# Kernel tuning notes

Hardware: AMD Instinct MI355X
Metric: run time of the kernel (lower is better)

The kernel has to match this reference:

```python
import jax, jax.numpy as jnp
import numpy as np
from jax import lax

B, T, HW = 8, 32, 128
D, NH, DEPTH, DFF = 384, 6, 6, 1536
PR = PC = 4
P = PR * PC
EPS = 1e-5


def _ln(x, g, b):
    mu = x.mean(-1, keepdims=True)
    v = ((x - mu) ** 2).mean(-1, keepdims=True)
    return (x - mu) / jnp.sqrt(v + EPS) * g + b


def _conv2d(x, w, s, p):
    return lax.conv_general_dilated(x, w, (s, s), [(p, p), (p, p)],
                                    dimension_numbers=('NCHW', 'OIHW', 'NCHW'))


def _bn(x, g, b, m, v):
    inv = g / jnp.sqrt(v + EPS)
    return x * inv[:, None, None] + (b - m * inv)[:, None, None]


def _gelu(x):
    return jax.nn.gelu(x, approximate=False)


def _forward(frames, conv1_w, bn1_g, bn1_b, bn1_m, bn1_v,
             conv2_w, bn2_g, bn2_b, bn2_m, bn2_v,
             conv3_w, bn3_g, bn3_b, bn3_m, bn3_v, proj_w,
             dw_w, dw_b, pw_w, pw_b, tnorm_g, tnorm_b,
             frame_pos, patch_pos, cls_token, cls_pos,
             qkv_w, qkv_b, out_w, out_b, ln1_g, ln1_b, ln2_g, ln2_b,
             ffn_w1, ffn_b1, ffn_w2, ffn_b2,
             head_ln_g, head_ln_b, head_w1, head_b1, head_w2, head_b2):
    b, t = frames.shape[0], frames.shape[1]
    # ---- FrameEncoder (eval-mode BN) ----
    x = frames.reshape(b * t, 1, HW, HW)
    x = _gelu(_bn(_conv2d(x, conv1_w, 2, 2), bn1_g, bn1_b, bn1_m, bn1_v))
    x = _gelu(_bn(_conv2d(x, conv2_w, 2, 1), bn2_g, bn2_b, bn2_m, bn2_v))
    x = _gelu(_bn(_conv2d(x, conv3_w, 2, 1), bn3_g, bn3_b, bn3_m, bn3_v))
    n, c, hh, ww = x.shape
    # adaptive avg pool (16,16)->(4,4) is an exact 4x4 mean pool
    x = x.reshape(n, c, PR, hh // PR, PC, ww // PC).mean(axis=(3, 5))
    x = jnp.einsum('oc,nchw->nohw', proj_w[:, :, 0, 0], x)  # 1x1 conv proj
    tokens = x.reshape(n, D, P).transpose(0, 2, 1).reshape(b, t, P, D)
    # ---- TemporalConvBlock (per-patch sequences) ----
    tc = tokens.transpose(0, 2, 1, 3).reshape(b * P, t, D)
    out = tc.transpose(0, 2, 1)  # [N, D, t]
    for i, dil in enumerate((1, 2)):
        pad = dil * (3 - 1) // 2
        h = lax.conv_general_dilated(out, dw_w[i], (1,), [(pad, pad)],
                                     rhs_dilation=(dil,), feature_group_count=D,
                                     dimension_numbers=('NCH', 'OIH', 'NCH'))
        h = _gelu(h + dw_b[i][None, :, None])
        h = jnp.einsum('oi,nit->not', pw_w[i], h) + pw_b[i][None, :, None]
        out = h + out
    out = out.transpose(0, 2, 1)
    tc = _ln(out + tc, tnorm_g, tnorm_b)
    tokens = tc.reshape(b, P, t, D).transpose(0, 2, 1, 3)
    # ---- positional + cls ----
    fp = frame_pos[:t].transpose(1, 0, 2)[:, :, None, :]  # [1,t,1,D]
    pp = patch_pos[:, None, :, :]                          # [1,1,P,D]
    tok = (tokens + fp + pp).reshape(b, t * P, D)
    cls = cls_token + cls_pos
    tok = jnp.concatenate([jnp.broadcast_to(cls, (b, 1, D)), tok], axis=1)
    S = t * P + 1
    # ---- block-structured additive mask (faithful to _build_causal_mask) ----
    ids = jnp.repeat(jnp.arange(t), P)
    neg = jnp.finfo(jnp.float32).min
    base = jnp.where(ids[None, :] < ids[:, None], neg, 0.0)
    mask = jnp.zeros((S, S), jnp.float32).at[1:, 1:].set(base).at[1:, 0].set(neg)
    # ---- pre-norm transformer encoder ----
    hd = D // NH
    scale = 1.0 / jnp.sqrt(jnp.float32(hd))
    x = tok
    for i in range(DEPTH):
        h = _ln(x, ln1_g[i], ln1_b[i])
        qkv = h @ qkv_w[i].T + qkv_b[i]
        q, k, v = jnp.split(qkv, 3, axis=-1)
        q = q.reshape(b, S, NH, hd).transpose(0, 2, 1, 3)
        k = k.reshape(b, S, NH, hd).transpose(0, 2, 1, 3)
        v = v.reshape(b, S, NH, hd).transpose(0, 2, 1, 3)
        scores = jnp.einsum('bhqd,bhkd->bhqk', q, k) * scale + mask
        a = jax.nn.softmax(scores, axis=-1)
        o = jnp.einsum('bhqk,bhkd->bhqd', a, v).transpose(0, 2, 1, 3).reshape(b, S, D)
        x = x + (o @ out_w[i].T + out_b[i])
        h2 = _ln(x, ln2_g[i], ln2_b[i])
        x = x + _gelu(h2 @ ffn_w1[i].T + ffn_b1[i]) @ ffn_w2[i].T + ffn_b2[i]
    # ---- coord head ----
    pooled = x[:, 0]
    h = _ln(pooled, head_ln_g, head_ln_b)
    h = _gelu(h @ head_w1.T + head_b1)
    coords = jax.nn.sigmoid(h @ head_w2.T + head_b2)
    return coords


def setup_inputs():
    ks = iter(jax.random.split(jax.random.key(0), 64))

    def r(shape, s):
        return jax.random.normal(next(ks), shape, jnp.float32) * s

    inp = {}
    inp['frames'] = jax.random.normal(next(ks), (B, T, 1, HW, HW), jnp.float32)
    inp['conv1_w'] = r((32, 1, 5, 5), 0.2)
    inp['bn1_g'] = jnp.ones(32); inp['bn1_b'] = jnp.zeros(32)
    inp['bn1_m'] = r((32,), 0.1)
    inp['bn1_v'] = jax.random.uniform(next(ks), (32,), jnp.float32, 0.5, 1.5)
    inp['conv2_w'] = r((64, 32, 3, 3), 0.1)
    inp['bn2_g'] = jnp.ones(64); inp['bn2_b'] = jnp.zeros(64)
    inp['bn2_m'] = r((64,), 0.1)
    inp['bn2_v'] = jax.random.uniform(next(ks), (64,), jnp.float32, 0.5, 1.5)
    inp['conv3_w'] = r((128, 64, 3, 3), 0.07)
    inp['bn3_g'] = jnp.ones(128); inp['bn3_b'] = jnp.zeros(128)
    inp['bn3_m'] = r((128,), 0.1)
    inp['bn3_v'] = jax.random.uniform(next(ks), (128,), jnp.float32, 0.5, 1.5)
    inp['proj_w'] = r((D, 128, 1, 1), 0.08)
    inp['dw_w'] = r((2, D, 1, 3), 0.3)
    inp['dw_b'] = jnp.zeros((2, D))
    inp['pw_w'] = r((2, D, D), 0.05)
    inp['pw_b'] = jnp.zeros((2, D))
    inp['tnorm_g'] = jnp.ones(D); inp['tnorm_b'] = jnp.zeros(D)
    inp['frame_pos'] = r((T, 1, D), 0.02)
    inp['patch_pos'] = r((1, P, D), 0.02)
    inp['cls_token'] = jnp.zeros((1, 1, D))
    inp['cls_pos'] = r((1, 1, D), 0.02)
    inp['qkv_w'] = r((DEPTH, 3 * D, D), 0.02)
    inp['qkv_b'] = jnp.zeros((DEPTH, 3 * D))
    inp['out_w'] = r((DEPTH, D, D), 0.02)
    inp['out_b'] = jnp.zeros((DEPTH, D))
    inp['ln1_g'] = jnp.ones((DEPTH, D)); inp['ln1_b'] = jnp.zeros((DEPTH, D))
    inp['ln2_g'] = jnp.ones((DEPTH, D)); inp['ln2_b'] = jnp.zeros((DEPTH, D))
    inp['ffn_w1'] = r((DEPTH, DFF, D), 0.02)
    inp['ffn_b1'] = jnp.zeros((DEPTH, DFF))
    inp['ffn_w2'] = r((DEPTH, D, DFF), 0.02)
    inp['ffn_b2'] = jnp.zeros((DEPTH, D))
    inp['head_ln_g'] = jnp.ones(D); inp['head_ln_b'] = jnp.zeros(D)
    inp['head_w1'] = r((D, D), 0.02); inp['head_b1'] = jnp.zeros(D)
    inp['head_w2'] = r((2, D), 0.02); inp['head_b2'] = jnp.zeros(2)
    return inp


def reference(frames, conv1_w, bn1_g, bn1_b, bn1_m, bn1_v,
              conv2_w, bn2_g, bn2_b, bn2_m, bn2_v,
              conv3_w, bn3_g, bn3_b, bn3_m, bn3_v, proj_w,
              dw_w, dw_b, pw_w, pw_b, tnorm_g, tnorm_b,
              frame_pos, patch_pos, cls_token, cls_pos,
              qkv_w, qkv_b, out_w, out_b, ln1_g, ln1_b, ln2_g, ln2_b,
              ffn_w1, ffn_b1, ffn_w2, ffn_b2,
              head_ln_g, head_ln_b, head_w1, head_b1, head_w2, head_b2):
    return _forward(frames, conv1_w, bn1_g, bn1_b, bn1_m, bn1_v,
                    conv2_w, bn2_g, bn2_b, bn2_m, bn2_v,
                    conv3_w, bn3_g, bn3_b, bn3_m, bn3_v, proj_w,
                    dw_w, dw_b, pw_w, pw_b, tnorm_g, tnorm_b,
                    frame_pos, patch_pos, cls_token, cls_pos,
                    qkv_w, qkv_b, out_w, out_b, ln1_g, ln1_b, ln2_g, ln2_b,
                    ffn_w1, ffn_b1, ffn_w2, ffn_b2,
                    head_ln_g, head_ln_b, head_w1, head_b1, head_w2, head_b2)
```

## Files before the change

kernel.cpp:

```cpp
#include <hip/hip_runtime.h>
#include <hip/hip_fp16.h>
#include <cstddef>

#define EPSV 1e-5f

typedef _Float16 f16;
typedef _Float16 f16x8 __attribute__((ext_vector_type(8)));
typedef float f32x4v __attribute__((ext_vector_type(4)));

__device__ __forceinline__ float gelu_f(float x) {
    return 0.5f * x * (1.0f + erff(x * 0.7071067811865476f));
}

__device__ __forceinline__ float gelu_fast(float x) {
    float y = 0.7978845608f * (x + 0.044715f * x * x * x);
    y = fminf(fmaxf(y, -10.f), 10.f);
    float e = __expf(2.f * y);
    float t = (e - 1.f) / (e + 1.f);
    return 0.5f * x * (1.f + t);
}

__global__ __launch_bounds__(256) void cvt_all_kernel(
    const float* __restrict__ p0, const float* __restrict__ p1,
    const float* __restrict__ p2, const float* __restrict__ p3,
    const float* __restrict__ p4, const float* __restrict__ p5,
    f16* __restrict__ dst)
{
    const int n = 10960896;
    for (int i = blockIdx.x * 256 + threadIdx.x; i < n; i += gridDim.x * 256) {
        const float* s; int off;
        if      (i <   49152) { s = p0; off = i; }
        else if (i <  344064) { s = p1; off = i -   49152; }
        else if (i < 2998272) { s = p2; off = i -  344064; }
        else if (i < 3883008) { s = p3; off = i - 2998272; }
        else if (i < 7421952) { s = p4; off = i - 3883008; }
        else                  { s = p5; off = i - 7421952; }
        dst[i] = (f16)s[off];
    }
}

__global__ __launch_bounds__(256) void conv_w_reorder_kernel(
    const float* __restrict__ w, f16* __restrict__ out, int CO, int CI)
{
    int n = CO * CI * 9;
    for (int i = blockIdx.x * 256 + threadIdx.x; i < n; i += gridDim.x * 256) {
        int t = i % 9; int r = i / 9;
        int ci = r % CI; int co = r / CI;
        out[(size_t)co * CI * 9 + t * CI + ci] = (f16)w[i];
    }
}

__global__ __launch_bounds__(256) void conv1_w_prep_kernel(
    const float* __restrict__ w, const float* __restrict__ g,
    const float* __restrict__ vr, f16* __restrict__ wB)
{
    int i = blockIdx.x * 256 + threadIdx.x;
    if (i >= 1024) return;
    int co = i >> 5, k = i & 31;
    float inv = g[co] * rsqrtf(vr[co] + EPSV);
    wB[i] = (f16)((k < 25) ? w[co * 25 + k] * inv : 0.f);
}

__global__ __launch_bounds__(256) void conv1_mfma_kernel(
    const float* __restrict__ in, const f16* __restrict__ wB,
    const float* __restrict__ bt, const float* __restrict__ mn,
    const float* __restrict__ g, const float* __restrict__ vr,
    f16* __restrict__ out)
{
    __shared__ __align__(16) f16 inpH[35 * 36 + 8];
    __shared__ __align__(16) f16 Bs[32 * 32];
    int bid = blockIdx.x;
    int n = bid >> 4; int tile = bid & 15;
    int ty0 = (tile >> 2) * 16, tx0 = (tile & 3) * 16;
    int t = threadIdx.x;
    const float* ip = in + (size_t)n * 16384;
    for (int e = t; e < 35 * 36; e += 256) {
        int r = e / 36, c = e - r * 36;
        int iy = ty0 * 2 - 2 + r, ix = tx0 * 2 - 2 + c;
        float v = ((unsigned)iy < 128u && (unsigned)ix < 128u && c < 35) ? ip[iy * 128 + ix] : 0.f;
        inpH[e] = (f16)v;
    }
    if (t < 128) {
        int row = t >> 2, seg = (t & 3) * 8;
        *(uint4*)(&Bs[row * 32 + seg]) = *(const uint4*)(wB + row * 32 + seg);
    }
    __syncthreads();
    int w = t >> 6, lane = t & 63;
    int l15 = lane & 15, gq = lane >> 4;
    f16x8 afr[4];
    #pragma unroll
    for (int i = 0; i < 4; i++) {
        int mt = 4 * w + i;
        f16 tmp[8];
        #pragma unroll
        for (int e = 0; e < 8; e++) {
            int kk = 8 * gq + e; if (kk > 24) kk = 24;
            int ky = kk / 5, kx = kk - ky * 5;
            tmp[e] = inpH[(2 * mt + ky) * 36 + 2 * l15 + kx];
        }
        afr[i] = *(f16x8*)tmp;
    }
    f16x8 bfr[2];
    bfr[0] = *(const f16x8*)(&Bs[l15 * 32 + 8 * gq]);
    bfr[1] = *(const f16x8*)(&Bs[(16 + l15) * 32 + 8 * gq]);
    f32x4v zero = {0.f, 0.f, 0.f, 0.f};
    f32x4v acc[4][2];
    #pragma unroll
    for (int i = 0; i < 4; i++) { acc[i][0] = zero; acc[i][1] = zero; }
    #pragma unroll
    for (int i = 0; i < 4; i++) {
        acc[i][0] = __builtin_amdgcn_mfma_f32_16x16x32_f16(afr[i], bfr[0], acc[i][0], 0, 0, 0);
        acc[i][1] = __builtin_amdgcn_mfma_f32_16x16x32_f16(afr[i], bfr[1], acc[i][1], 0, 0, 0);
    }
    float beta[2];
    #pragma unroll
    for (int nt = 0; nt < 2; nt++) {
        int co = nt * 16 + l15;
        float inv = g[co] * rsqrtf(vr[co] + EPSV);
        beta[nt] = bt[co] - mn[co] * inv;
    }
    #pragma unroll
    for (int i = 0; i < 4; i++) {
        int y = ty0 + 4 * w + i;
        #pragma unroll
        for (int q = 0; q < 4; q++) {
            int x = tx0 + 4 * gq + q;
            size_t ob = (((size_t)n * 64 + y) * 64 + x) * 32;
            #pragma unroll
            for (int nt = 0; nt < 2; nt++) {
                int co = nt * 16 + l15;
                out[ob + co] = (f16)gelu_fast(acc[i][nt][q] + beta[nt]);
            }
        }
    }
}

template<int CI, int HI, int CO>
__global__ __launch_bounds__(256) void convg_kernel(
    const f16* __restrict__ in, const f16* __restrict__ wr_,
    const float* __restrict__ g, const float* __restrict__ bt,
    const float* __restrict__ mn, const float* __restrict__ vr,
    f16* __restrict__ out)
{
    constexpr int HO = HI / 2;
    constexpr int HOB = (HO == 32) ? 5 : 4;
    constexpr int K = 9 * CI;
    __shared__ __align__(16) f16 As[64 * 40];
    __shared__ __align__(16) f16 Bs[64 * 40];
    int tid = threadIdx.x;
    int bm = blockIdx.x * 64;
    int bn = blockIdx.y * 64;
    int lrow = tid >> 2, lseg = tid & 3;
    int w = tid >> 6, lane = tid & 63;
    int wr = (w >> 1) * 32, wc = (w & 1) * 32;
    int l15 = lane & 15, l4 = lane >> 4;
    int gp = bm + lrow;
    int pn = gp >> (2 * HOB);
    int prem = gp & ((1 << (2 * HOB)) - 1);
    int oy = prem >> HOB, ox = prem & (HO - 1);

    f32x4v zero = {0.f, 0.f, 0.f, 0.f};
    f32x4v acc[2][2];
    acc[0][0] = zero; acc[0][1] = zero; acc[1][0] = zero; acc[1][1] = zero;

    auto loadTile = [&](int k0, uint4& av, uint4& bv) {
        int tap = k0 / CI;
        int cio = k0 - tap * CI;
        int ky = tap / 3, kx = tap - ky * 3;
        int iy = oy * 2 - 1 + ky, ix = ox * 2 - 1 + kx;
        av = make_uint4(0u, 0u, 0u, 0u);
        if ((unsigned)iy < (unsigned)HI && (unsigned)ix < (unsigned)HI)
            av = *(const uint4*)(in + (((size_t)(pn * HI + iy)) * HI + ix) * CI + cio + lseg * 8);
        bv = *(const uint4*)(wr_ + (size_t)(bn + lrow) * K + k0 + lseg * 8);
    };

    uint4 ra, rb;
    loadTile(0, ra, rb);
    for (int k0 = 0; k0 < K; k0 += 32) {
        __syncthreads();
        *(uint4*)(&As[lrow * 40 + lseg * 8]) = ra;
        *(uint4*)(&Bs[lrow * 40 + lseg * 8]) = rb;
        if (k0 + 32 < K) loadTile(k0 + 32, ra, rb);
        __syncthreads();
        f16x8 a0 = *(const f16x8*)(&As[(wr + l15) * 40 + l4 * 8]);
        f16x8 a1 = *(const f16x8*)(&As[(wr + 16 + l15) * 40 + l4 * 8]);
        f16x8 b0 = *(const f16x8*)(&Bs[(wc + l15) * 40 + l4 * 8]);
        f16x8 b1 = *(const f16x8*)(&Bs[(wc + 16 + l15) * 40 + l4 * 8]);
        acc[0][0] = __builtin_amdgcn_mfma_f32_16x16x32_f16(a0, b0, acc[0][0], 0, 0, 0);
        acc[0][1] = __builtin_amdgcn_mfma_f32_16x16x32_f16(a0, b1, acc[0][1], 0, 0, 0);
        acc[1][0] = __builtin_amdgcn_mfma_f32_16x16x32_f16(a1, b0, acc[1][0], 0, 0, 0);
        acc[1][1] = __builtin_amdgcn_mfma_f32_16x16x32_f16(a1, b1, acc[1][1], 0, 0, 0);
    }
    float inv[2], beta[2];
    #pragma unroll
    for (int ni = 0; ni < 2; ni++) {
        int col = bn + wc + ni * 16 + l15;
        float iv = g[col] * rsqrtf(vr[col] + EPSV);
        inv[ni] = iv; beta[ni] = bt[col] - mn[col] * iv;
    }
    #pragma unroll
    for (int mi = 0; mi < 2; mi++) {
        #pragma unroll
        for (int q = 0; q < 4; q++) {
            int pixel = bm + wr + mi * 16 + l4 * 4 + q;
            #pragma unroll
            for (int ni = 0; ni < 2; ni++) {
                int col = bn + wc + ni * 16 + l15;
                float v = acc[mi][ni][q] * inv[ni] + beta[ni];
                out[(size_t)pixel * CO + col] = (f16)gelu_fast(v);
            }
        }
    }
}

__global__ __launch_bounds__(256) void poolh_kernel(
    const f16* __restrict__ in, f16* __restrict__ out, int NC)
{
    int idx = blockIdx.x * 256 + threadIdx.x;
    if (idx >= NC * 16 * 16) return;
    int cc = idx & 15; int npl = idx >> 4;
    int c0 = cc * 8;
    int n = npl >> 4; int p = npl & 15;
    int ph = p >> 2, pw = p & 3;
    const f16* base = in + (((size_t)(n * 16 + ph * 4)) * 16 + pw * 4) * 128 + c0;
    float s[8] = {};
    #pragma unroll
    for (int dy = 0; dy < 4; dy++)
        #pragma unroll
        for (int dx = 0; dx < 4; dx++) {
            f16x8 v = *(const f16x8*)(base + (dy * 16 + dx) * 128);
            #pragma unroll
            for (int u = 0; u < 8; u++) s[u] += (float)v[u];
        }
    f16* op = out + (size_t)npl * 128 + c0;
    #pragma unroll
    for (int u = 0; u < 8; u++) op[u] = (f16)(s[u] * 0.0625f);
}

template<int OUTF16, int ACT, int VTRANS>
__global__ __launch_bounds__(256) void gemm_k64_kernel(
    const f16* __restrict__ A, const f16* __restrict__ B,
    const float* __restrict__ bias, const float* __restrict__ res,
    void* __restrict__ Cv, f16* __restrict__ vT, int M, int N, int K, int nrow)
{
    __shared__ __align__(16) f16 As[64 * 72];
    __shared__ __align__(16) f16 Bs[64 * 72];
    int nb = gridDim.x;
    int q = nb >> 3, r = nb & 7;
    int xcd = blockIdx.x & 7, pos = blockIdx.x >> 3;
    int logical = (xcd < r ? xcd * (q + 1) : r * (q + 1) + (xcd - r) * q) + pos;
    int brow = logical % nrow, bcol = logical / nrow;
    int bm = brow * 64, bn = bcol * 64;

    int tid = threadIdx.x;
    int lrow = tid >> 2, lseg = (tid & 3) * 16;
    int w = tid >> 6, lane = tid & 63;
    int wr = (w >> 1) * 32, wc = (w & 1) * 32;
    int l15 = lane & 15, l4 = lane >> 4;
    f32x4v zero = {0.f, 0.f, 0.f, 0.f};
    f32x4v acc[2][2];
    acc[0][0] = zero; acc[0][1] = zero; acc[1][0] = zero; acc[1][1] = zero;

    int arow = bm + lrow;
    bool aok = (arow < M);
    const f16* ap = A + (size_t)arow * K + lseg;
    const f16* bp = B + (size_t)(bn + lrow) * K + lseg;

    uint4 ra0 = make_uint4(0u,0u,0u,0u), ra1 = ra0, rb0, rb1;
    if (aok) { ra0 = *(const uint4*)(ap); ra1 = *(const uint4*)(ap + 8); }
    rb0 = *(const uint4*)(bp); rb1 = *(const uint4*)(bp + 8);

    int nt = K >> 6;
    for (int t = 0; t < nt; t++) {
        __syncthreads();
        *(uint4*)(&As[lrow * 72 + lseg])     = ra0;
        *(uint4*)(&As[lrow * 72 + lseg + 8]) = ra1;
        *(uint4*)(&Bs[lrow * 72 + lseg])     = rb0;
        *(uint4*)(&Bs[lrow * 72 + lseg + 8]) = rb1;
        if (t + 1 < nt) {
            int k0 = (t + 1) << 6;
            if (aok) { ra0 = *(const uint4*)(ap + k0); ra1 = *(const uint4*)(ap + k0 + 8); }
            rb0 = *(const uint4*)(bp + k0); rb1 = *(const uint4*)(bp + k0 + 8);
        }
        __syncthreads();
        #pragma unroll
        for (int s = 0; s < 2; s++) {
            f16x8 a0 = *(const f16x8*)(&As[(wr + l15) * 72 + s * 32 + l4 * 8]);
            f16x8 a1 = *(const f16x8*)(&As[(wr + 16 + l15) * 72 + s * 32 + l4 * 8]);
            f16x8 b0 = *(const f16x8*)(&Bs[(wc + l15) * 72 + s * 32 + l4 * 8]);
            f16x8 b1 = *(const f16x8*)(&Bs[(wc + 16 + l15) * 72 + s * 32 + l4 * 8]);
            acc[0][0] = __builtin_amdgcn_mfma_f32_16x16x32_f16(a0, b0, acc[0][0], 0, 0, 0);
            acc[0][1] = __builtin_amdgcn_mfma_f32_16x16x32_f16(a0, b1, acc[0][1], 0, 0, 0);
            acc[1][0] = __builtin_amdgcn_mfma_f32_16x16x32_f16(a1, b0, acc[1][0], 0, 0, 0);
            acc[1][1] = __builtin_amdgcn_mfma_f32_16x16x32_f16(a1, b1, acc[1][1], 0, 0, 0);
        }
    }

    if (VTRANS && bn >= 768) {
        __syncthreads();
        f16* tile = As;
        #pragma unroll
        for (int mi = 0; mi < 2; mi++)
            #pragma unroll
            for (int qq = 0; qq < 4; qq++) {
                int rl = wr + mi * 16 + l4 * 4 + qq;
                #pragma unroll
                for (int ni = 0; ni < 2; ni++) {
                    int dl = wc + ni * 16 + l15;
                    float v = acc[mi][ni][qq] + bias[bn + dl];
                    tile[dl * 66 + rl] = (f16)v;
                }
            }
        __syncthreads();
        int h = (bn - 768) >> 6;
        int j = tid & 63, dbase = tid >> 6;
        int trow = bm + j;
        if (trow < M) {
            int b = trow / 513;
            int jj = trow - b * 513;
            f16* vb = vT + ((size_t)(b * 6 + h) * 64) * 576 + jj;
            #pragma unroll
            for (int it = 0; it < 16; it++) {
                int d = dbase * 16 + it;
                vb[(size_t)d * 576] = tile[d * 66 + j];
            }
        }
        return;
    }
    #pragma unroll
    for (int mi = 0; mi < 2; mi++) {
        #pragma unroll
        for (int qq = 0; qq < 4; qq++) {
            int row = bm + wr + mi * 16 + l4 * 4 + qq;
            if (row >= M) continue;
            #pragma unroll
            for (int ni = 0; ni < 2; ni++) {
                int col = bn + wc + ni * 16 + l15;
                float v = acc[mi][ni][qq];
                if (bias) v += bias[col];
                if (ACT == 1) v = gelu_fast(v);
                if (res) v += res[(size_t)row * N + col];
                if (OUTF16) ((f16*)Cv)[(size_t)row * N + col] = (f16)v;
                else ((float*)Cv)[(size_t)row * N + col] = v;
            }
        }
    }
}

template<int ACT>
__global__ __launch_bounds__(256) void gemm_kn128_kernel(
    const f16* __restrict__ A, const f16* __restrict__ B,
    const float* __restrict__ bias, f16* __restrict__ C,
    int M, int N, int K, int nrow)
{
    __shared__ __align__(16) f16 As[64 * 72];
    __shared__ __align__(16) f16 Bs[128 * 72];
    int nb = gridDim.x;
    int q = nb >> 3, r = nb & 7;
    int xcd = blockIdx.x & 7, pos = blockIdx.x >> 3;
    int logical = (xcd < r ? xcd * (q + 1) : r * (q + 1) + (xcd - r) * q) + pos;
    int brow = logical % nrow, bcol = logical / nrow;
    int bm = brow * 64, bn = bcol * 128;

    int tid = threadIdx.x;
    int w = tid >> 6, lane = tid & 63;
    int wr = (w >> 1) * 32, wc = (w & 1) * 64;
    int l15 = lane & 15, l4 = lane >> 4;
    int alrow = tid >> 2, alseg = (tid & 3) * 16;
    int blrow = tid >> 1, blseg = (tid & 1) * 32;

    f32x4v zero = {0.f, 0.f, 0.f, 0.f};
    f32x4v acc[2][4];
    #pragma unroll
    for (int i = 0; i < 2; i++)
        #pragma unroll
        for (int j = 0; j < 4; j++) acc[i][j] = zero;

    int arow = bm + alrow;
    bool aok = (arow < M);
    const f16* ap = A + (size_t)arow * K + alseg;
    const f16* bp = B + (size_t)(bn + blrow) * K + blseg;

    uint4 ra0 = make_uint4(0u,0u,0u,0u), ra1 = ra0;
    uint4 rb0, rb1, rb2, rb3;
    if (aok) { ra0 = *(const uint4*)(ap); ra1 = *(const uint4*)(ap + 8); }
    rb0 = *(const uint4*)(bp);      rb1 = *(const uint4*)(bp + 8);
    rb2 = *(const uint4*)(bp + 16); rb3 = *(const uint4*)(bp + 24);

    int ntiles = K >> 6;
    for (int t = 0; t < ntiles; t++) {
        __syncthreads();
        *(uint4*)(&As[alrow * 72 + alseg])     = ra0;
        *(uint4*)(&As[alrow * 72 + alseg + 8]) = ra1;
        *(uint4*)(&Bs[blrow * 72 + blseg])      = rb0;
        *(uint4*)(&Bs[blrow * 72 + blseg + 8])  = rb1;
        *(uint4*)(&Bs[blrow * 72 + blseg + 16]) = rb2;
        *(uint4*)(&Bs[blrow * 72 + blseg + 24]) = rb3;
        if (t + 1 < ntiles) {
            int k0 = (t + 1) << 6;
            if (aok) { ra0 = *(const uint4*)(ap + k0); ra1 = *(const uint4*)(ap + k0 + 8); }
            rb0 = *(const uint4*)(bp + k0);      rb1 = *(const uint4*)(bp + k0 + 8);
            rb2 = *(const uint4*)(bp + k0 + 16); rb3 = *(const uint4*)(bp + k0 + 24);
        }
        __syncthreads();
        #pragma unroll
        for (int s = 0; s < 2; s++) {
            f16x8 a0 = *(const f16x8*)(&As[(wr + l15) * 72 + s * 32 + l4 * 8]);
            f16x8 a1 = *(const f16x8*)(&As[(wr + 16 + l15) * 72 + s * 32 + l4 * 8]);
            #pragma unroll
            for (int j = 0; j < 4; j++) {
                f16x8 bf = *(const f16x8*)(&Bs[(wc + j * 16 + l15) * 72 + s * 32 + l4 * 8]);
                acc[0][j] = __builtin_amdgcn_mfma_f32_16x16x32_f16(a0, bf, acc[0][j], 0, 0, 0);
                acc[1][j] = __builtin_amdgcn_mfma_f32_16x16x32_f16(a1, bf, acc[1][j], 0, 0, 0);
            }
        }
    }
    #pragma unroll
    for (int mi = 0; mi < 2; mi++) {
        #pragma unroll
        for (int qq = 0; qq < 4; qq++) {
            int row = bm + wr + mi * 16 + l4 * 4 + qq;
            if (row >= M) continue;
            #pragma unroll
            for (int j = 0; j < 4; j++) {
                int col = bn + wc + j * 16 + l15;
                float v = acc[mi][j][qq];
                if (bias) v += bias[col];
                if (ACT == 1) v = gelu_fast(v);
                C[(size_t)row * N + col] = (f16)v;
            }
        }
    }
}

__global__ __launch_bounds__(256) void tok2tc_kernel(
    const float* __restrict__ in, float* __restrict__ out)
{
    int idx = blockIdx.x * 256 + threadIdx.x;
    if (idx >= 8 * 32 * 16 * 384) return;
    int d = idx % 384; int t2 = idx / 384;
    int p = t2 & 15; t2 >>= 4;
    int t = t2 & 31; int b = t2 >> 5;
    out[(((size_t)(b * 16 + p) * 32 + t) * 384) + d] = in[idx];
}

__global__ __launch_bounds__(256) void dwconv_kernel(
    const float* __restrict__ in, const float* __restrict__ w,
    const float* __restrict__ bias, f16* __restrict__ out, int dil)
{
    int idx = blockIdx.x * 256 + threadIdx.x;
    if (idx >= 128 * 32 * 384) return;
    int d = idx % 384; int t = (idx / 384) & 31; int s = idx / (384 * 32);
    const float* ip = in + (size_t)s * 32 * 384 + d;
    float acc = bias[d];
    #pragma unroll
    for (int k = 0; k < 3; k++) {
        int tt = t + (k - 1) * dil;
        if ((unsigned)tt < 32u) acc += w[d * 3 + k] * ip[tt * 384];
    }
    out[idx] = (f16)gelu_fast(acc);
}

__global__ __launch_bounds__(256) void ln_wave_kernel(
    const float* __restrict__ in,
    const float* __restrict__ g, const float* __restrict__ b,
    f16* __restrict__ out, int rows)
{
    int w = threadIdx.x >> 6, lane = threadIdx.x & 63;
    int row = blockIdx.x * 4 + w;
    if (row >= rows) return;
    const float* ip = in + (size_t)row * 384;
    float x[6]; float s = 0.f, s2 = 0.f;
    #pragma unroll
    for (int k = 0; k < 6; k++) {
        float v = ip[lane + 64 * k];
        x[k] = v; s += v; s2 += v * v;
    }
    #pragma unroll
    for (int off = 1; off < 64; off <<= 1) {
        s += __shfl_xor(s, off); s2 += __shfl_xor(s2, off);
    }
    float mu = s * (1.f / 384.f);
    float var = s2 * (1.f / 384.f) - mu * mu;
    float rs = rsqrtf(var + EPSV);
    #pragma unroll
    for (int k = 0; k < 6; k++) {
        int c = lane + 64 * k;
        out[(size_t)row * 384 + c] = (f16)((x[k] - mu) * rs * g[c] + b[c]);
    }
}

__global__ __launch_bounds__(128) void build_x_kernel(
    const float* __restrict__ mix, const float* __restrict__ tc,
    const float* __restrict__ tg, const float* __restrict__ tb,
    const float* __restrict__ fpos, const float* __restrict__ ppos,
    float* __restrict__ x)
{
    int row = blockIdx.x;
    int t = row & 31; int bp = row >> 5;
    int p = bp & 15; int b = bp >> 4;
    int tid = threadIdx.x;
    const float* ip = mix + (size_t)row * 384;
    const float* ip2 = tc + (size_t)row * 384;
    __shared__ float red[128], red2[128];
    float v[3]; float s = 0.f, s2 = 0.f;
    #pragma unroll
    for (int j = 0; j < 3; j++) {
        float val = ip[tid + 128 * j] + ip2[tid + 128 * j];
        v[j] = val; s += val; s2 += val * val;
    }
    red[tid] = s; red2[tid] = s2; __syncthreads();
    for (int off = 64; off >= 1; off >>= 1) {
        if (tid < off) { red[tid] += red[tid + off]; red2[tid] += red2[tid + off]; }
        __syncthreads();
    }
    float mu = red[0] * (1.f / 384.f);
    float var = red2[0] * (1.f / 384.f) - mu * mu;
    float rs = rsqrtf(var + EPSV);
    size_t xbase = ((size_t)b * 513 + 1 + t * 16 + p) * 384;
    #pragma unroll
    for (int j = 0; j < 3; j++) {
        int c = tid + 128 * j;
        float y = (v[j] - mu) * rs * tg[c] + tb[c] + fpos[t * 384 + c] + ppos[p * 384 + c];
        x[xbase + c] = y;
    }
}

__global__ __launch_bounds__(256) void cls_kernel(
    const float* __restrict__ ct, const float* __restrict__ cp, float* __restrict__ x)
{
    int idx = blockIdx.x * 256 + threadIdx.x;
    if (idx >= 8 * 384) return;
    int c = idx % 384; int b = idx / 384;
    x[(size_t)b * 513 * 384 + c] = ct[c] + cp[c];
}

__global__ __launch_bounds__(256) void fattn_split_kernel(
    const f16* __restrict__ qkv, const f16* __restrict__ vT,
    f16* __restrict__ Op, float* __restrict__ ml)
{
    __shared__ __align__(16) f16 Pl[4][16][72];
    int qt = blockIdx.x;
    int bh = blockIdx.y; int h = bh % 6; int b = bh / 6;
    int third = blockIdx.z;
    int tid = threadIdx.x;
    int w = tid >> 6, lane = tid & 63;
    int l15 = lane & 15, g = lane >> 4;
    int q0w = qt * 64 + w * 16;
    if (q0w > 512) return;
    const size_t RS = 1152;
    const f16* qbase = qkv + (size_t)b * 513 * RS + h * 64;
    const f16* kbase = qbase + 384;
    const f16* vtb = vT + (size_t)bh * 64 * 576;

    f16x8 qf[2];
    {
        int qrow = q0w + l15; if (qrow > 512) qrow = 512;
        const f16* qp = qbase + (size_t)qrow * RS + g * 8;
        qf[0] = *(const f16x8*)(qp);
        qf[1] = *(const f16x8*)(qp + 32);
    }

    f32x4v zero = {0.f, 0.f, 0.f, 0.f};
    f32x4v O[4]; float m[4], l[4];
    #pragma unroll
    for (int i = 0; i < 4; i++) { O[i] = zero; m[i] = -INFINITY; l[i] = 0.f; }

    int jt0 = 0;
    if (q0w > 0) { int fmin = (q0w - 1) >> 4; jt0 = (fmin * 16 + 1) >> 6; }

    int jrow[4];
    #pragma unroll
    for (int jf = 0; jf < 4; jf++) jrow[jf] = jf * 16 + l15;

    auto loadK = [&](int j0, f16x8* kr) {
        #pragma unroll
        for (int s = 0; s < 2; s++)
            #pragma unroll
            for (int jf = 0; jf < 4; jf++) {
                int j = j0 + jrow[jf]; if (j > 512) j = 512;
                kr[s * 4 + jf] = *(const f16x8*)(kbase + (size_t)j * RS + s * 32 + g * 8);
            }
    };

    int jt = jt0 + third;
    f16x8 kreg[8];
    if (jt < 9) loadK(jt * 64, kreg);

    for (; jt < 9; jt += 3) {
        int j0 = jt * 64;
        f16x8 vreg[8];
        #pragma unroll
        for (int s = 0; s < 2; s++)
            #pragma unroll
            for (int df = 0; df < 4; df++)
                vreg[s * 4 + df] = *(const f16x8*)(vtb + (size_t)(df * 16 + l15) * 576 + j0 + s * 32 + g * 8);
        f32x4v S[4];
        #pragma unroll
        for (int jf = 0; jf < 4; jf++) S[jf] = zero;
        #pragma unroll
        for (int s = 0; s < 2; s++)
            #pragma unroll
            for (int jf = 0; jf < 4; jf++)
                S[jf] = __builtin_amdgcn_mfma_f32_16x16x32_f16(qf[s], kreg[s * 4 + jf], S[jf], 0, 0, 0);
        f16x8 knext[8];
        if (jt + 3 < 9) loadK((jt + 3) * 64, knext);
        float pj[4][4];
        #pragma unroll
        for (int r = 0; r < 4; r++) {
            int qi = q0w + 4 * g + r;
            int fi = (qi == 0) ? -1 : ((qi - 1) >> 4);
            float mx = -INFINITY;
            #pragma unroll
            for (int jf = 0; jf < 4; jf++) {
                int j = j0 + jrow[jf];
                bool valid = (qi < 513) && (j < 513) &&
                             !((qi != 0) && ((j == 0) || (((j - 1) >> 4) < fi)));
                float sv = valid ? S[jf][r] * 0.125f : -INFINITY;
                pj[jf][r] = sv;
                mx = fmaxf(mx, sv);
            }
            mx = fmaxf(mx, __shfl_xor(mx, 1));
            mx = fmaxf(mx, __shfl_xor(mx, 2));
            mx = fmaxf(mx, __shfl_xor(mx, 4));
            mx = fmaxf(mx, __shfl_xor(mx, 8));
            float mn = fmaxf(m[r], mx);
            float alpha = (m[r] == -INFINITY) ? 0.f : __expf(m[r] - mn);
            float ls = 0.f;
            #pragma unroll
            for (int jf = 0; jf < 4; jf++) {
                float p = (pj[jf][r] == -INFINITY) ? 0.f : __expf(pj[jf][r] - mn);
                pj[jf][r] = p; ls += p;
            }
            ls += __shfl_xor(ls, 1); ls += __shfl_xor(ls, 2);
            ls += __shfl_xor(ls, 4); ls += __shfl_xor(ls, 8);
            l[r] = alpha * l[r] + ls;
            m[r] = mn;
            #pragma unroll
            for (int df = 0; df < 4; df++) O[df][r] *= alpha;
        }
        #pragma unroll
        for (int jf = 0; jf < 4; jf++)
            #pragma unroll
            for (int r = 0; r < 4; r++)
                Pl[w][4 * g + r][jf * 16 + l15] = (f16)pj[jf][r];
        #pragma unroll
        for (int s = 0; s < 2; s++) {
            f16x8 pf = *(const f16x8*)(&Pl[w][l15][s * 32 + g * 8]);
            #pragma unroll
            for (int df = 0; df < 4; df++)
                O[df] = __builtin_amdgcn_mfma_f32_16x16x32_f16(pf, vreg[s * 4 + df], O[df], 0, 0, 0);
        }
        #pragma unroll
        for (int i = 0; i < 8; i++) kreg[i] = knext[i];
    }

    int rowbase = third * 24624 + bh * 513;
    #pragma unroll
    for (int r = 0; r < 4; r++) {
        int qi = q0w + 4 * g + r;
        if (qi > 512) continue;
        size_t ro = (size_t)(rowbase + qi);
        #pragma unroll
        for (int df = 0; df < 4; df++)
            Op[ro * 64 + df * 16 + l15] = (f16)O[df][r];
        if (l15 == 0) {
            ml[ro * 2 + 0] = m[r];
            ml[ro * 2 + 1] = l[r];
        }
    }
}

__global__ __launch_bounds__(256) void attn_combine_kernel(
    const f16* __restrict__ Op, const float* __restrict__ ml,
    f16* __restrict__ ob)
{
    int row = blockIdx.x * 4 + (threadIdx.x >> 6);
    if (row >= 24624) return;
    int lane = threadIdx.x & 63;
    int bh = row / 513, qi = row - bh * 513;
    int b = bh / 6, h = bh - b * 6;
    float mv[3], lv[3], mm = -INFINITY;
    #pragma unroll
    for (int s = 0; s < 3; s++) {
        mv[s] = ml[((size_t)s * 24624 + row) * 2];
        lv[s] = ml[((size_t)s * 24624 + row) * 2 + 1];
        mm = fmaxf(mm, mv[s]);
    }
    float onum = 0.f, lden = 0.f;
    #pragma unroll
    for (int s = 0; s < 3; s++) {
        float a = (mv[s] == -INFINITY) ? 0.f : __expf(mv[s] - mm);
        lden += lv[s] * a;
        onum += (float)Op[((size_t)s * 24624 + row) * 64 + lane] * a;
    }
    ob[((size_t)(b * 513 + qi)) * 384 + h * 64 + lane] = (f16)(onum / lden);
}

__global__ __launch_bounds__(384) void head_kernel(
    const float* __restrict__ x, const float* __restrict__ lg, const float* __restrict__ lb,
    const float* __restrict__ w1, const float* __restrict__ b1,
    const float* __restrict__ w2, const float* __restrict__ b2,
    float* __restrict__ out)
{
    int b = blockIdx.x; int t = threadIdx.x;
    __shared__ float hs[384], h1[384];
    __shared__ float rs[6], rs2[6];
    const float* xp = x + (size_t)b * 513 * 384;
    float v = xp[t];
    float s = v, s2 = v * v;
    #pragma unroll
    for (int off = 32; off >= 1; off >>= 1) {
        s += __shfl_down(s, off); s2 += __shfl_down(s2, off);
    }
    if ((t & 63) == 0) { rs[t >> 6] = s; rs2[t >> 6] = s2; }
    __syncthreads();
    float S = 0.f, S2 = 0.f;
    #pragma unroll
    for (int i = 0; i < 6; i++) { S += rs[i]; S2 += rs2[i]; }
    float mu = S * (1.f / 384.f);
    float var = S2 * (1.f / 384.f) - mu * mu;
    float rstd = rsqrtf(var + EPSV);
    hs[t] = (v - mu) * rstd * lg[t] + lb[t];
    __syncthreads();
    const float* wr = w1 + (size_t)t * 384;
    float acc = b1[t];
    for (int c = 0; c < 384; c += 4) {
        float4 w4 = *reinterpret_cast<const float4*>(wr + c);
        acc += w4.x * hs[c] + w4.y * hs[c + 1] + w4.z * hs[c + 2] + w4.w * hs[c + 3];
    }
    h1[t] = gelu_f(acc);
    __syncthreads();
    float p0 = h1[t] * w2[t], p1 = h1[t] * w2[384 + t];
    #pragma unroll
    for (int off = 32; off >= 1; off >>= 1) {
        p0 += __shfl_down(p0, off); p1 += __shfl_down(p1, off);
    }
    if ((t & 63) == 0) { rs[t >> 6] = p0; rs2[t >> 6] = p1; }
    __syncthreads();
    if (t == 0) {
        float a0 = b2[0], a1 = b2[1];
        #pragma unroll
        for (int i = 0; i < 6; i++) { a0 += rs[i]; a1 += rs2[i]; }
        out[b * 2 + 0] = 1.f / (1.f + expf(-a0));
        out[b * 2 + 1] = 1.f / (1.f + expf(-a1));
    }
}

static inline int cdiv(int a, int b) { return (a + b - 1) / b; }

extern "C" void kernel_launch(void* const* d_in, const int* in_sizes, int n_in,
                              void* d_out, int out_size, void* d_ws, size_t ws_size,
                              hipStream_t stream)
{
    const float* frames  = (const float*)d_in[0];
    const float* conv1_w = (const float*)d_in[1];
    const float* bn1_g = (const float*)d_in[2]; const float* bn1_b = (const float*)d_in[3];
    const float* bn1_m = (const float*)d_in[4]; const float* bn1_v = (const float*)d_in[5];
    const float* conv2_w = (const float*)d_in[6];
    const float* bn2_g = (const float*)d_in[7]; const float* bn2_b = (const float*)d_in[8];
    const float* bn2_m = (const float*)d_in[9]; const float* bn2_v = (const float*)d_in[10];
    const float* conv3_w = (const float*)d_in[11];
    const float* bn3_g = (const float*)d_in[12]; const float* bn3_b = (const float*)d_in[13];
    const float* bn3_m = (const float*)d_in[14]; const float* bn3_v = (const float*)d_in[15];
    const float* proj_w = (const float*)d_in[16];
    const float* dw_w = (const float*)d_in[17]; const float* dw_b = (const float*)d_in[18];
    const float* pw_w = (const float*)d_in[19]; const float* pw_b = (const float*)d_in[20];
    const float* tnorm_g = (const float*)d_in[21]; const float* tnorm_b = (const float*)d_in[22];
    const float* frame_pos = (const float*)d_in[23];
    const float* patch_pos = (const float*)d_in[24];
    const float* cls_token = (const float*)d_in[25];
    const float* cls_pos = (const float*)d_in[26];
    const float* qkv_w = (const float*)d_in[27]; const float* qkv_b = (const float*)d_in[28];
    const float* out_w = (const float*)d_in[29]; const float* out_b = (const float*)d_in[30];
    const float* ln1_g = (const float*)d_in[31]; const float* ln1_b = (const float*)d_in[32];
    const float* ln2_g = (const float*)d_in[33]; const float* ln2_b = (const float*)d_in[34];
    const float* ffn_w1 = (const float*)d_in[35]; const float* ffn_b1 = (const float*)d_in[36];
    const float* ffn_w2 = (const float*)d_in[37]; const float* ffn_b2 = (const float*)d_in[38];
    const float* head_ln_g = (const float*)d_in[39]; const float* head_ln_b = (const float*)d_in[40];
    const float* head_w1 = (const float*)d_in[41]; const float* head_b1 = (const float*)d_in[42];
    const float* head_w2 = (const float*)d_in[43]; const float* head_b2 = (const float*)d_in[44];
    (void)in_sizes; (void)n_in; (void)out_size; (void)ws_size;

    char* base = (char*)d_ws;
    size_t off = 0;
    auto alloc = [&](size_t bytes) { void* p = base + off; off = (off + bytes + 255) & ~(size_t)255; return p; };

    f16* wtotal = (f16*)alloc((size_t)10960896 * 2);
    f16* projw16 = wtotal;
    f16* pw16    = wtotal + 49152;
    f16* qkvw16  = wtotal + 344064;
    f16* outw16  = wtotal + 2998272;
    f16* f1w16   = wtotal + 3883008;
    f16* f2w16   = wtotal + 7421952;
    f16* c1wB    = (f16*)alloc(1024 * 2);
    f16* c2w16   = (f16*)alloc((size_t)64 * 288 * 2);
    f16* c3w16   = (f16*)alloc((size_t)128 * 576 * 2);
    float* tokens = (float*)alloc((size_t)4096 * 384 * 4);
    f16* pooled   = (f16*)alloc((size_t)4096 * 128 * 2);

    size_t ustart = off;
    f16* c1h = (f16*)alloc((size_t)256 * 64 * 64 * 32 * 2);
    f16* c2h = (f16*)alloc((size_t)256 * 32 * 32 * 64 * 2);
    f16* c3h = (f16*)alloc((size_t)256 * 16 * 16 * 128 * 2);
    size_t uend_stem = off;
    off = ustart;
    float* tc = (float*)alloc((size_t)4096 * 384 * 4);
    float* mA = (float*)alloc((size_t)4096 * 384 * 4);
    float* mB = (float*)alloc((size_t)4096 * 384 * 4);
    f16*   mh = (f16*)alloc((size_t)4096 * 384 * 2);
    float* xb   = (float*)alloc((size_t)8 * 513 * 384 * 4);
    f16*   hb   = (f16*)alloc((size_t)8 * 513 * 384 * 2);
    f16*   qkvb = (f16*)alloc((size_t)8 * 513 * 1152 * 2);
    f16*   vTb  = (f16*)alloc((size_t)48 * 64 * 576 * 2);
    f16*   ob   = (f16*)alloc((size_t)8 * 513 * 384 * 2);
    f16*   ffb  = (f16*)alloc((size_t)8 * 513 * 1536 * 2);
    f16*   Opart = (f16*)alloc((size_t)3 * 24624 * 64 * 2);
    float* mlpart = (float*)alloc((size_t)3 * 24624 * 2 * 4);
    if (off < uend_stem) off = uend_stem;

    cvt_all_kernel<<<4096, 256, 0, stream>>>(
        proj_w, pw_w, qkv_w, out_w, ffn_w1, ffn_w2, wtotal);
    conv1_w_prep_kernel<<<4, 256, 0, stream>>>(conv1_w, bn1_g, bn1_v, c1wB);
    conv_w_reorder_kernel<<<cdiv(64 * 288, 256), 256, 0, stream>>>(conv2_w, c2w16, 64, 32);
    conv_w_reorder_kernel<<<cdiv(128 * 576, 256), 256, 0, stream>>>(conv3_w, c3w16, 128, 64);

    conv1_mfma_kernel<<<256 * 16, 256, 0, stream>>>(
        frames, c1wB, bn1_b, bn1_m, bn1_g, bn1_v, c1h);
    convg_kernel<32, 64, 64><<<dim3(4096, 1), 256, 0, stream>>>(
        c1h, c2w16, bn2_g, bn2_b, bn2_m, bn2_v, c2h);
    convg_kernel<64, 32, 128><<<dim3(1024, 2), 256, 0, stream>>>(
        c2h, c3w16, bn3_g, bn3_b, bn3_m, bn3_v, c3h);
    poolh_kernel<<<256, 256, 0, stream>>>(c3h, pooled, 256);
    gemm_k64_kernel<0, 0, 0><<<384, 256, 0, stream>>>(
        pooled, projw16, nullptr, nullptr, tokens, nullptr, 4096, 384, 128, 64);

    tok2tc_kernel<<<cdiv(8 * 32 * 16 * 384, 256), 256, 0, stream>>>(tokens, tc);
    dwconv_kernel<<<cdiv(128 * 32 * 384, 256), 256, 0, stream>>>(
        tc, dw_w, dw_b, mh, 1);
    gemm_k64_kernel<0, 0, 0><<<384, 256, 0, stream>>>(
        mh, pw16, pw_b, tc, mA, nullptr, 4096, 384, 384, 64);
    dwconv_kernel<<<cdiv(128 * 32 * 384, 256), 256, 0, stream>>>(
        mA, dw_w + 384 * 3, dw_b + 384, mh, 2);
    gemm_k64_kernel<0, 0, 0><<<384, 256, 0, stream>>>(
        mh, pw16 + 384 * 384, pw_b + 384, mA, mB, nullptr, 4096, 384, 384, 64);

    build_x_kernel<<<128 * 32, 128, 0, stream>>>(
        mB, tc, tnorm_g, tnorm_b, frame_pos, patch_pos, xb);
    cls_kernel<<<cdiv(8 * 384, 256), 256, 0, stream>>>(cls_token, cls_pos, xb);

    const int M = 8 * 513;
    const int NR = cdiv(M, 64);
    for (int l = 0; l < 6; l++) {
        ln_wave_kernel<<<cdiv(M, 4), 256, 0, stream>>>(xb,
            ln1_g + (size_t)l * 384, ln1_b + (size_t)l * 384, hb, M);
        gemm_k64_kernel<1, 0, 1><<<NR * 18, 256, 0, stream>>>(
            hb, qkvw16 + (size_t)l * 1152 * 384, qkv_b + (size_t)l * 1152,
            nullptr, qkvb, vTb, M, 1152, 384, NR);
        fattn_split_kernel<<<dim3(9, 48, 3), 256, 0, stream>>>(qkvb, vTb, Opart, mlpart);
        attn_combine_kernel<<<cdiv(24624, 4), 256, 0, stream>>>(Opart, mlpart, ob);
        gemm_k64_kernel<0, 0, 0><<<NR * 6, 256, 0, stream>>>(
            ob, outw16 + (size_t)l * 384 * 384, out_b + (size_t)l * 384,
            xb, xb, nullptr, M, 384, 384, NR);
        ln_wave_kernel<<<cdiv(M, 4), 256, 0, stream>>>(xb,
            ln2_g + (size_t)l * 384, ln2_b + (size_t)l * 384, hb, M);
        gemm_kn128_kernel<1><<<NR * 12, 256, 0, stream>>>(
            hb, f1w16 + (size_t)l * 1536 * 384, ffn_b1 + (size_t)l * 1536,
            ffb, M, 1536, 384, NR);
        gemm_k64_kernel<0, 0, 0><<<NR * 6, 256, 0, stream>>>(
            ffb, f2w16 + (size_t)l * 384 * 1536, ffn_b2 + (size_t)l * 384,
            xb, xb, nullptr, M, 384, 1536, NR);
    }

    head_kernel<<<8, 384, 0, stream>>>(
        xb, head_ln_g, head_ln_b, head_w1, head_b1, head_w2, head_b2, (float*)d_out);
}
```

Baseline: 851.0 us.

## Fuse token transpose into proj GEMM, cheaper GELU, four attention splits

The projection GEMM now writes its output directly in the per-patch temporal layout through a row remap, which removes the separate tok2tc transpose kernel and one full buffer round-trip. The tanh-approximate GELU is rewritten as x*sigmoid(1.702-ish polynomial) using exp2 and a hardware reciprocal, cutting ALU work in the GEMM and dwconv epilogues. Flash-attention key splits go from 3 to 4, giving more blocks for parallelism at the cost of extra partial outputs for the combine step. The row remap relies on the exact 4096-row tiling, and the GELU rewrite drops the input clamp, so very large inputs rely on exp2 saturating to infinity.

```diff
diff --git a/kernel.cpp b/kernel.cpp
--- a/kernel.cpp
+++ b/kernel.cpp
@@ -3,6 +3,7 @@
 #include <cstddef>
 
 #define EPSV 1e-5f
+#define SPLITS 4
 
 typedef _Float16 f16;
 typedef _Float16 f16x8 __attribute__((ext_vector_type(8)));
@@ -13,11 +14,11 @@
 }
 
 __device__ __forceinline__ float gelu_fast(float x) {
-    float y = 0.7978845608f * (x + 0.044715f * x * x * x);
-    y = fminf(fmaxf(y, -10.f), 10.f);
-    float e = __expf(2.f * y);
-    float t = (e - 1.f) / (e + 1.f);
-    return 0.5f * x * (1.f + t);
+    float x2 = x * x;
+    float z = x * fmaf(0.10296103f, x2, 2.3025851f);
+    float e = exp2f(z);
+    float r = __builtin_amdgcn_rcpf(e + 1.0f);
+    return fmaf(-x, r, x);
 }
 
 __global__ __launch_bounds__(256) void cvt_all_kernel(
@@ -237,7 +238,7 @@
     for (int u = 0; u < 8; u++) op[u] = (f16)(s[u] * 0.0625f);
 }
 
-template<int OUTF16, int ACT, int VTRANS>
+template<int OUTF16, int ACT, int VTRANS, int TCMAP>
 __global__ __launch_bounds__(256) void gemm_k64_kernel(
     const f16* __restrict__ A, const f16* __restrict__ B,
     const float* __restrict__ bias, const float* __restrict__ res,
@@ -340,8 +341,10 @@
                 if (bias) v += bias[col];
                 if (ACT == 1) v = gelu_fast(v);
                 if (res) v += res[(size_t)row * N + col];
-                if (OUTF16) ((f16*)Cv)[(size_t)row * N + col] = (f16)v;
-                else ((float*)Cv)[(size_t)row * N + col] = v;
+                int orow = row;
+                if (TCMAP) orow = (row & ~511) | ((row & 15) << 5) | ((row >> 4) & 31);
+                if (OUTF16) ((f16*)Cv)[(size_t)orow * N + col] = (f16)v;
+                else ((float*)Cv)[(size_t)orow * N + col] = v;
             }
         }
     }
@@ -433,17 +436,6 @@
     }
 }
 
-__global__ __launch_bounds__(256) void tok2tc_kernel(
-    const float* __restrict__ in, float* __restrict__ out)
-{
-    int idx = blockIdx.x * 256 + threadIdx.x;
-    if (idx >= 8 * 32 * 16 * 384) return;
-    int d = idx % 384; int t2 = idx / 384;
-    int p = t2 & 15; t2 >>= 4;
-    int t = t2 & 31; int b = t2 >> 5;
-    out[(((size_t)(b * 16 + p) * 32 + t) * 384) + d] = in[idx];
-}
-
 __global__ __launch_bounds__(256) void dwconv_kernel(
     const float* __restrict__ in, const float* __restrict__ w,
     const float* __restrict__ bias, f16* __restrict__ out, int dil)
@@ -587,7 +579,7 @@
     f16x8 kreg[8];
     if (jt < 9) loadK(jt * 64, kreg);
 
-    for (; jt < 9; jt += 3) {
+    for (; jt < 9; jt += SPLITS) {
         int j0 = jt * 64;
         f16x8 vreg[8];
         #pragma unroll
@@ -604,7 +596,7 @@
             for (int jf = 0; jf < 4; jf++)
                 S[jf] = __builtin_amdgcn_mfma_f32_16x16x32_f16(qf[s], kreg[s * 4 + jf], S[jf], 0, 0, 0);
         f16x8 knext[8];
-        if (jt + 3 < 9) loadK((jt + 3) * 64, knext);
+        if (jt + SPLITS < 9) loadK((jt + SPLITS) * 64, knext);
         float pj[4][4];
         #pragma unroll
         for (int r = 0; r < 4; r++) {
@@ -680,16 +672,16 @@
     int lane = threadIdx.x & 63;
     int bh = row / 513, qi = row - bh * 513;
     int b = bh / 6, h = bh - b * 6;
-    float mv[3], lv[3], mm = -INFINITY;
-    #pragma unroll
-    for (int s = 0; s < 3; s++) {
+    float mv[SPLITS], lv[SPLITS], mm = -INFINITY;
+    #pragma unroll
+    for (int s = 0; s < SPLITS; s++) {
         mv[s] = ml[((size_t)s * 24624 + row) * 2];
         lv[s] = ml[((size_t)s * 24624 + row) * 2 + 1];
         mm = fmaxf(mm, mv[s]);
     }
     float onum = 0.f, lden = 0.f;
     #pragma unroll
-    for (int s = 0; s < 3; s++) {
+    for (int s = 0; s < SPLITS; s++) {
         float a = (mv[s] == -INFINITY) ? 0.f : __expf(mv[s] - mm);
         lden += lv[s] * a;
         onum += (float)Op[((size_t)s * 24624 + row) * 64 + lane] * a;
@@ -796,8 +788,8 @@
     f16* c1wB    = (f16*)alloc(1024 * 2);
     f16* c2w16   = (f16*)alloc((size_t)64 * 288 * 2);
     f16* c3w16   = (f16*)alloc((size_t)128 * 576 * 2);
-    float* tokens = (float*)alloc((size_t)4096 * 384 * 4);
-    f16* pooled   = (f16*)alloc((size_t)4096 * 128 * 2);
+    f16* pooled  = (f16*)alloc((size_t)4096 * 128 * 2);
+    float* tc    = (float*)alloc((size_t)4096 * 384 * 4);
 
     size_t ustart = off;
     f16* c1h = (f16*)alloc((size_t)256 * 64 * 64 * 32 * 2);
@@ -805,7 +797,6 @@
     f16* c3h = (f16*)alloc((size_t)256 * 16 * 16 * 128 * 2);
     size_t uend_stem = off;
     off = ustart;
-    float* tc = (float*)alloc((size_t)4096 * 384 * 4);
     float* mA = (float*)alloc((size_t)4096 * 384 * 4);
     float* mB = (float*)alloc((size_t)4096 * 384 * 4);
     f16*   mh = (f16*)alloc((size_t)4096 * 384 * 2);
@@ -815,8 +806,8 @@
     f16*   vTb  = (f16*)alloc((size_t)48 * 64 * 576 * 2);
     f16*   ob   = (f16*)alloc((size_t)8 * 513 * 384 * 2);
     f16*   ffb  = (f16*)alloc((size_t)8 * 513 * 1536 * 2);
-    f16*   Opart = (f16*)alloc((size_t)3 * 24624 * 64 * 2);
-    float* mlpart = (float*)alloc((size_t)3 * 24624 * 2 * 4);
+    f16*   Opart = (f16*)alloc((size_t)SPLITS * 24624 * 64 * 2);
+    float* mlpart = (float*)alloc((size_t)SPLITS * 24624 * 2 * 4);
     if (off < uend_stem) off = uend_stem;
 
     cvt_all_kernel<<<4096, 256, 0, stream>>>(
@@ -832,17 +823,16 @@
     convg_kernel<64, 32, 128><<<dim3(1024, 2), 256, 0, stream>>>(
         c2h, c3w16, bn3_g, bn3_b, bn3_m, bn3_v, c3h);
     poolh_kernel<<<256, 256, 0, stream>>>(c3h, pooled, 256);
-    gemm_k64_kernel<0, 0, 0><<<384, 256, 0, stream>>>(
-        pooled, projw16, nullptr, nullptr, tokens, nullptr, 4096, 384, 128, 64);
-
-    tok2tc_kernel<<<cdiv(8 * 32 * 16 * 384, 256), 256, 0, stream>>>(tokens, tc);
+    gemm_k64_kernel<0, 0, 0, 1><<<384, 256, 0, stream>>>(
+        pooled, projw16, nullptr, nullptr, tc, nullptr, 4096, 384, 128, 64);
+
     dwconv_kernel<<<cdiv(128 * 32 * 384, 256), 256, 0, stream>>>(
         tc, dw_w, dw_b, mh, 1);
-    gemm_k64_kernel<0, 0, 0><<<384, 256, 0, stream>>>(
+    gemm_k64_kernel<0, 0, 0, 0><<<384, 256, 0, stream>>>(
         mh, pw16, pw_b, tc, mA, nullptr, 4096, 384, 384, 64);
     dwconv_kernel<<<cdiv(128 * 32 * 384, 256), 256, 0, stream>>>(
         mA, dw_w + 384 * 3, dw_b + 384, mh, 2);
-    gemm_k64_kernel<0, 0, 0><<<384, 256, 0, stream>>>(
+    gemm_k64_kernel<0, 0, 0, 0><<<384, 256, 0, stream>>>(
         mh, pw16 + 384 * 384, pw_b + 384, mA, mB, nullptr, 4096, 384, 384, 64);
 
     build_x_kernel<<<128 * 32, 128, 0, stream>>>(
@@ -854,12 +844,12 @@
     for (int l = 0; l < 6; l++) {
         ln_wave_kernel<<<cdiv(M, 4), 256, 0, stream>>>(xb,
             ln1_g + (size_t)l * 384, ln1_b + (size_t)l * 384, hb, M);
-        gemm_k64_kernel<1, 0, 1><<<NR * 18, 256, 0, stream>>>(
+        gemm_k64_kernel<1, 0, 1, 0><<<NR * 18, 256, 0, stream>>>(
             hb, qkvw16 + (size_t)l * 1152 * 384, qkv_b + (size_t)l * 1152,
             nullptr, qkvb, vTb, M, 1152, 384, NR);
-        fattn_split_kernel<<<dim3(9, 48, 3), 256, 0, stream>>>(qkvb, vTb, Opart, mlpart);
+        fattn_split_kernel<<<dim3(9, 48, SPLITS), 256, 0, stream>>>(qkvb, vTb, Opart, mlpart);
         attn_combine_kernel<<<cdiv(24624, 4), 256, 0, stream>>>(Opart, mlpart, ob);
-        gemm_k64_kernel<0, 0, 0><<<NR * 6, 256, 0, stream>>>(
+        gemm_k64_kernel<0, 0, 0, 0><<<NR * 6, 256, 0, stream>>>(
             ob, outw16 + (size_t)l * 384 * 384, out_b + (size_t)l * 384,
             xb, xb, nullptr, M, 384, 384, NR);
         ln_wave_kernel<<<cdiv(M, 4), 256, 0, stream>>>(xb,
@@ -867,7 +857,7 @@
         gemm_kn128_kernel<1><<<NR * 12, 256, 0, stream>>>(
             hb, f1w16 + (size_t)l * 1536 * 384, ffn_b1 + (size_t)l * 1536,
             ffb, M, 1536, 384, NR);
-        gemm_k64_kernel<0, 0, 0><<<NR * 6, 256, 0, stream>>>(
+        gemm_k64_kernel<0, 0, 0, 0><<<NR * 6, 256, 0, stream>>>(
             ffb, f2w16 + (size_t)l * 384 * 1536, ffn_b2 + (size_t)l * 384,
             xb, xb, nullptr, M, 384, 1536, NR);
     }
```

Measured after the change: 836.0 us. About the same (-1.8%).
